# Optimization experiments

Hardware: AMD Instinct MI355X
Metric: run time of the kernel (lower is better)

Reference implementation:

```python
import jax, jax.numpy as jnp
import numpy as np

B, S, D = 4, 2048, 1024
H = 16
HD = D // H  # head dim = 64


def setup_inputs() -> dict:
    key = jax.random.key(0)
    ks = jax.random.split(key, 9)
    s = 1.0 / np.sqrt(D)
    return {
        "Q": jax.random.normal(ks[0], (B, S, D), dtype=jnp.float32),
        "K": jax.random.normal(ks[1], (B, S, D), dtype=jnp.float32),
        "V": jax.random.normal(ks[2], (B, S, D), dtype=jnp.float32),
        "Wq": jax.random.uniform(ks[3], (D, D), jnp.float32, -s, s),
        "bq": jax.random.uniform(ks[4], (D,), jnp.float32, -s, s),
        "Wk": jax.random.uniform(ks[5], (D, D), jnp.float32, -s, s),
        "bk": jax.random.uniform(ks[6], (D,), jnp.float32, -s, s),
        "Wv": jax.random.uniform(ks[7], (D, D), jnp.float32, -s, s),
        "bv": jax.random.uniform(ks[8], (D,), jnp.float32, -s, s),
    }


def reference(Q, K, V, Wq, bq, Wk, bk, Wv, bv):
    # Linear projections, split into heads: (B, H, S, HD)
    def proj(x, W, b):
        y = x @ W + b  # torch Linear uses x @ W.T; here W is stored pre-transposed (D_in, D_out)
        return y.reshape(B, S, H, HD).transpose(0, 2, 1, 3)

    q = proj(Q, Wq, bq)
    k = proj(K, Wk, bk)
    v = proj(V, Wv, bv)

    scale = 1.0 / jnp.sqrt(jnp.float32(HD))
    scores = jnp.einsum("bhqd,bhkd->bhqk", q, k) * scale  # (B,H,S,S)
    # causal mask (mask=True path): -inf above the diagonal
    causal = jnp.triu(jnp.full((S, S), -jnp.inf, dtype=scores.dtype), k=1)
    scores = scores + causal
    attn = jax.nn.softmax(scores, axis=-1)
    ctx = jnp.einsum("bhqk,bhkd->bhqd", attn, v)  # (B,H,S,HD)
    return ctx.transpose(0, 2, 1, 3).reshape(B, S, H * HD)
```

## Files before the change

kernel.cpp:

```cpp
#include <hip/hip_runtime.h>
#include <hip/hip_bf16.h>
#include <stdint.h>

#define B_  4
#define S_  2048
#define D_  1024
#define H_  16
#define HD_ 64
#define LOG2E 1.44269504088896f

typedef unsigned short u16;
typedef short bf16x8 __attribute__((ext_vector_type(8)));
typedef float f32x4 __attribute__((ext_vector_type(4)));

static __device__ __forceinline__ u16 f2bf(float f) {
    union { float f; uint32_t u; } v; v.f = f;
    return (u16)((v.u + 0x7FFF + ((v.u >> 16) & 1)) >> 16);
}

static __device__ __forceinline__ uint32_t cvt_pk_bf16(float lo, float hi) {
    uint32_t r;
    asm("v_cvt_pk_bf16_f32 %0, %1, %2" : "=v"(r) : "v"(lo), "v"(hi));
    return r;
}

static __device__ __forceinline__ uint32_t pk2(float lo, float hi) {
    return __builtin_amdgcn_perm(__float_as_uint(hi), __float_as_uint(lo), 0x07060302u);
}

static __device__ __forceinline__ bf16x8 rd_swz(const u16* base, int row, int slot) {
    return *(const bf16x8*)((const char*)base + row * 128 + ((slot ^ (row & 7)) << 4));
}

static __device__ __forceinline__ void gll_swz(const u16* grow0, size_t stride,
                                               u16* lds_chunk, int lane) {
    const int r = lane >> 3;
    const int slot = (lane & 7) ^ r;
    const u16* g = grow0 + (size_t)r * stride + slot * 8;
    __builtin_amdgcn_global_load_lds(
        (const __attribute__((address_space(1))) uint32_t*)g,
        (__attribute__((address_space(3))) uint32_t*)lds_chunk, 16, 0, 0);
}

__global__ __launch_bounds__(256) void wtrans(
    const float* __restrict__ W0, const float* __restrict__ W1, const float* __restrict__ W2,
    u16* __restrict__ T0, u16* __restrict__ T1, u16* __restrict__ T2)
{
    const float* W = blockIdx.z == 0 ? W0 : (blockIdx.z == 1 ? W1 : W2);
    u16* T       = blockIdx.z == 0 ? T0 : (blockIdx.z == 1 ? T1 : T2);
    __shared__ float t[32][33];
    const int n0 = blockIdx.x * 32, k0 = blockIdx.y * 32;
    const int tx = threadIdx.x, ty = threadIdx.y;
#pragma unroll
    for (int i = 0; i < 4; ++i)
        t[ty + i * 8][tx] = W[(size_t)(k0 + ty + i * 8) * D_ + n0 + tx];
    __syncthreads();
#pragma unroll
    for (int i = 0; i < 4; ++i)
        T[(size_t)(n0 + ty + i * 8) * D_ + k0 + tx] = f2bf(t[tx][ty + i * 8]);
}

template <int MODE>
__global__ __launch_bounds__(256) void proj_gemm(
    const float* __restrict__ X, const u16* __restrict__ Wt,
    const float* __restrict__ bias, u16* __restrict__ out)
{
    __shared__ __align__(16) u16 lA[2][128 * 64];
    __shared__ __align__(16) u16 lB[2][128 * 64];
    const int tid = threadIdx.x;
    const int m0 = blockIdx.x * 128, n0 = blockIdx.y * 128;
    const int w = tid >> 6, lane = tid & 63;
    const int lr = lane & 15, lg = lane >> 4;
    const int wr = (w >> 1) * 64, wc = (w & 1) * 64;

    f32x4 acc[4][4] = {};
    float4 areg[8];

    auto loadA = [&](int k0) {
#pragma unroll
        for (int i = 0; i < 4; ++i) {
            const int lin = (i * 256 + tid) * 8;
            const int r = lin >> 6, c = lin & 63;
            const float* p = X + (size_t)(m0 + r) * D_ + k0 + c;
            areg[2 * i]     = *(const float4*)p;
            areg[2 * i + 1] = *(const float4*)(p + 4);
        }
    };
    auto writeA = [&](u16* dst) {
#pragma unroll
        for (int i = 0; i < 4; ++i) {
            const int lin = (i * 256 + tid) * 8;
            const int r = lin >> 6, c = lin & 63;
            uint4 pk;
            pk.x = pk2(areg[2 * i].x,     areg[2 * i].y);
            pk.y = pk2(areg[2 * i].z,     areg[2 * i].w);
            pk.z = pk2(areg[2 * i + 1].x, areg[2 * i + 1].y);
            pk.w = pk2(areg[2 * i + 1].z, areg[2 * i + 1].w);
            const int phys = r * 128 + (((c >> 3) ^ (r & 7)) << 4);
            *(uint4*)((char*)dst + phys) = pk;
        }
    };
    auto stageB = [&](int k0, u16* dst) {
#pragma unroll
        for (int i = 0; i < 4; ++i) {
            const int c = w * 4 + i;
            gll_swz(Wt + (size_t)(n0 + c * 8) * D_ + k0, D_, dst + c * 512, lane);
        }
    };
    auto mfmaStep = [&](const u16* A, const u16* Bb) {
#pragma unroll
        for (int kk = 0; kk < 2; ++kk) {
            bf16x8 af[4], bfr[4];
#pragma unroll
            for (int m = 0; m < 4; ++m)
                af[m] = rd_swz(A, wr + m * 16 + lr, kk * 4 + lg);
#pragma unroll
            for (int n = 0; n < 4; ++n)
                bfr[n] = rd_swz(Bb, wc + n * 16 + lr, kk * 4 + lg);
#pragma unroll
            for (int m = 0; m < 4; ++m)
#pragma unroll
                for (int n = 0; n < 4; ++n)
                    acc[m][n] = __builtin_amdgcn_mfma_f32_16x16x32_bf16(af[m], bfr[n], acc[m][n], 0, 0, 0);
        }
    };

    loadA(0);
    stageB(0, lB[0]);
    writeA(lA[0]);
    __syncthreads();

    for (int k0 = 0, s = 0; k0 < D_; k0 += 64, s ^= 1) {
        const int nk = k0 + 64;
        if (nk < D_) {
            loadA(nk);
            stageB(nk, lB[s ^ 1]);
        }
        mfmaStep(lA[s], lB[s]);
        if (nk < D_) writeA(lA[s ^ 1]);
        __syncthreads();
    }

#pragma unroll
    for (int m = 0; m < 4; ++m)
#pragma unroll
        for (int n = 0; n < 4; ++n)
#pragma unroll
            for (int j = 0; j < 4; ++j) {
                const int gm = m0 + wr + m * 16 + lg * 4 + j;
                const int gn = n0 + wc + n * 16 + lr;
                float y = acc[m][n][j] + bias[gn];
                if (MODE == 0) y *= 0.125f * LOG2E;
                const int bb = gm >> 11, s2 = gm & (S_ - 1);
                const int h = gn >> 6, hd = gn & 63;
                size_t off;
                if (MODE < 2) off = (((size_t)bb * H_ + h) * S_ + s2) * HD_ + hd;
                else {
                    const int s6 = s2 & 63;
                    const int sp = (s2 & ~63) | (s6 & 0x20) | ((s6 & 0xC) << 1) |
                                   ((s6 & 0x10) >> 2) | (s6 & 3);
                    off = (((size_t)bb * H_ + h) * HD_ + hd) * S_ + sp;
                }
                out[off] = f2bf(y);
            }
}

__global__ __launch_bounds__(512) void attn_kernel(
    const u16* __restrict__ qb, const u16* __restrict__ kb,
    const u16* __restrict__ vtb, float* __restrict__ out)
{
    const int flat = (int)blockIdx.x;
    const int qA = flat >> 6;
    const int bh = ((flat & 7) << 3) | ((flat >> 3) & 7);
    const int b = bh >> 4, h = bh & 15;
    const int tid = threadIdx.x;
    const int w = tid >> 6, lane = tid & 63;
    const int lr = lane & 15, lg = lane >> 4;

    __shared__ __align__(16) u16 lds[2][4][64 * 64];

    const size_t kbase = (size_t)bh * S_ * HD_;
    const size_t vbase = (size_t)bh * HD_ * S_;

    union { uint32_t u[4]; bf16x8 v; } onesf;
    onesf.u[0] = onesf.u[1] = onesf.u[2] = onesf.u[3] = 0x3F803F80u;

    const int qB = 15 - qA;
    const int q0A = qA * 128, q0B = qB * 128;
    const int qrowA = q0A + w * 16 + lr;
    const int qrowB = q0B + w * 16 + lr;
    const int tmaxA = 2 * qA + 1, tmaxB = 2 * qB + 1;

    const size_t qoffA = ((size_t)bh * S_ + qrowA) * HD_;
    const size_t qoffB = ((size_t)bh * S_ + qrowB) * HD_;
    const bf16x8 qfA0 = *(const bf16x8*)(qb + qoffA + lg * 8);
    const bf16x8 qfA1 = *(const bf16x8*)(qb + qoffA + 32 + lg * 8);
    const bf16x8 qfB0 = *(const bf16x8*)(qb + qoffB + lg * 8);
    const bf16x8 qfB1 = *(const bf16x8*)(qb + qoffB + 32 + lg * 8);

    f32x4 oaccA[4] = {}, oaccB[4] = {};
    f32x4 laccA = {}, laccB = {};

    auto stage = [&](int tp, int s) {
        const int kvA = tp * 64, kvB = kvA + 64;
        u16* d = &lds[s][0][0];
        gll_swz(kb + kbase + (size_t)(kvA + w * 8) * HD_, HD_, d + w * 512, lane);
        gll_swz(vtb + vbase + (size_t)(w * 8) * S_ + kvA, S_, d + 4096 + w * 512, lane);
        gll_swz(kb + kbase + (size_t)(kvB + w * 8) * HD_, HD_, d + 8192 + w * 512, lane);
        gll_swz(vtb + vbase + (size_t)(w * 8) * S_ + kvB, S_, d + 12288 + w * 512, lane);
    };

    auto computeT = [&](int t, const u16* lK, const u16* lV,
                        const bf16x8& Qf0, const bf16x8& Qf1,
                        f32x4 (&oacc)[4], f32x4& lacc, int qrow, int tmax) {
        const int kv0 = t * 64;
        f32x4 sacc[4];
        __builtin_amdgcn_s_setprio(1);
#pragma unroll
        for (int n = 0; n < 4; ++n) {
            const bf16x8 k0f = rd_swz(lK, n * 16 + lr, lg);
            const bf16x8 k1f = rd_swz(lK, n * 16 + lr, 4 + lg);
            f32x4 z = {};
            z = __builtin_amdgcn_mfma_f32_16x16x32_bf16(k0f, Qf0, z, 0, 0, 0);
            z = __builtin_amdgcn_mfma_f32_16x16x32_bf16(k1f, Qf1, z, 0, 0, 0);
            sacc[n] = z;
        }
        __builtin_amdgcn_s_setprio(0);

        if (t >= tmax - 1) {
#pragma unroll
            for (int n = 0; n < 4; ++n)
#pragma unroll
                for (int j = 0; j < 4; ++j)
                    if (kv0 + n * 16 + lg * 4 + j > qrow) sacc[n][j] = -1e30f;
        }

        uint32_t pw[4][2];
#pragma unroll
        for (int n = 0; n < 4; ++n)
#pragma unroll
            for (int jh = 0; jh < 2; ++jh)
                pw[n][jh] = cvt_pk_bf16(exp2f(sacc[n][2 * jh]),
                                        exp2f(sacc[n][2 * jh + 1]));

        union { uint32_t u[4]; bf16x8 v; } a0, a1;
        a0.u[0] = pw[0][0]; a0.u[1] = pw[0][1];
        a0.u[2] = pw[1][0]; a0.u[3] = pw[1][1];
        a1.u[0] = pw[2][0]; a1.u[1] = pw[2][1];
        a1.u[2] = pw[3][0]; a1.u[3] = pw[3][1];

        __builtin_amdgcn_s_setprio(1);
#pragma unroll
        for (int n = 0; n < 4; ++n) {
            const int row = n * 16 + lr;
            const bf16x8 vf0 = rd_swz(lV, row, lg);
            const bf16x8 vf1 = rd_swz(lV, row, 4 + lg);
            oacc[n] = __builtin_amdgcn_mfma_f32_16x16x32_bf16(a0.v, vf0, oacc[n], 0, 0, 0);
            oacc[n] = __builtin_amdgcn_mfma_f32_16x16x32_bf16(a1.v, vf1, oacc[n], 0, 0, 0);
        }
        lacc = __builtin_amdgcn_mfma_f32_16x16x32_bf16(a0.v, onesf.v, lacc, 0, 0, 0);
        lacc = __builtin_amdgcn_mfma_f32_16x16x32_bf16(a1.v, onesf.v, lacc, 0, 0, 0);
        __builtin_amdgcn_s_setprio(0);
    };

    stage(0, 0);
    __syncthreads();

    for (int tp = 0, s = 0; tp <= tmaxB; tp += 2, s ^= 1) {
        if (tp + 2 <= tmaxB) stage(tp + 2, s ^ 1);
        const u16* base = &lds[s][0][0];

        computeT(tp, base, base + 4096, qfB0, qfB1, oaccB, laccB, qrowB, tmaxB);
        if (!(tp + 1 == tmaxB && w < 4))
            computeT(tp + 1, base + 8192, base + 12288, qfB0, qfB1, oaccB, laccB, qrowB, tmaxB);

        if (tp <= tmaxA) {
            computeT(tp, base, base + 4096, qfA0, qfA1, oaccA, laccA, qrowA, tmaxA);
            if (!(tp + 1 == tmaxA && w < 4))
                computeT(tp + 1, base + 8192, base + 12288, qfA0, qfA1, oaccA, laccA, qrowA, tmaxA);
        }
        __syncthreads();
    }

    {
        f32x4 inv;
#pragma unroll
        for (int j = 0; j < 4; ++j) inv[j] = 1.f / laccA[j];
#pragma unroll
        for (int j = 0; j < 4; ++j) {
            const int row = q0A + w * 16 + lg * 4 + j;
#pragma unroll
            for (int n = 0; n < 4; ++n)
                out[((size_t)b * S_ + row) * D_ + h * HD_ + n * 16 + lr] = oaccA[n][j] * inv[j];
        }
    }
    {
        f32x4 inv;
#pragma unroll
        for (int j = 0; j < 4; ++j) inv[j] = 1.f / laccB[j];
#pragma unroll
        for (int j = 0; j < 4; ++j) {
            const int row = q0B + w * 16 + lg * 4 + j;
#pragma unroll
            for (int n = 0; n < 4; ++n)
                out[((size_t)b * S_ + row) * D_ + h * HD_ + n * 16 + lr] = oaccB[n][j] * inv[j];
        }
    }
}

extern "C" void kernel_launch(void* const* d_in, const int* in_sizes, int n_in,
                              void* d_out, int out_size, void* d_ws, size_t ws_size,
                              hipStream_t stream) {
    const float* Q  = (const float*)d_in[0];
    const float* K  = (const float*)d_in[1];
    const float* V  = (const float*)d_in[2];
    const float* Wq = (const float*)d_in[3];
    const float* bq = (const float*)d_in[4];
    const float* Wk = (const float*)d_in[5];
    const float* bk = (const float*)d_in[6];
    const float* Wv = (const float*)d_in[7];
    const float* bv = (const float*)d_in[8];
    float* out = (float*)d_out;

    char* ws = (char*)d_ws;
    const size_t WT_BYTES  = (size_t)D_ * D_ * 2;
    const size_t QKV_BYTES = (size_t)B_ * S_ * D_ * 2;
    u16* Wtq = (u16*)(ws);
    u16* Wtk = (u16*)(ws + WT_BYTES);
    u16* Wtv = (u16*)(ws + 2 * WT_BYTES);
    u16* qb  = (u16*)(ws + 3 * WT_BYTES);
    u16* kb  = (u16*)(ws + 3 * WT_BYTES + QKV_BYTES);
    u16* vtb = (u16*)(ws + 3 * WT_BYTES + 2 * QKV_BYTES);

    wtrans<<<dim3(32, 32, 3), dim3(32, 8), 0, stream>>>(Wq, Wk, Wv, Wtq, Wtk, Wtv);
    proj_gemm<0><<<dim3(64, 8), dim3(256), 0, stream>>>(Q, Wtq, bq, qb);
    proj_gemm<1><<<dim3(64, 8), dim3(256), 0, stream>>>(K, Wtk, bk, kb);
    proj_gemm<2><<<dim3(64, 8), dim3(256), 0, stream>>>(V, Wtv, bv, vtb);
    attn_kernel<<<dim3(512), dim3(512), 0, stream>>>(qb, kb, vtb, out);
}
```

Baseline: 144.6 us.

## Deepen projection GEMM pipeline with register double-buffered A prefetch and partial vmcnt waits

```diff
diff --git a/kernel.cpp b/kernel.cpp
--- a/kernel.cpp
+++ b/kernel.cpp
@@ -59,6 +59,19 @@
     for (int i = 0; i < 4; ++i)
         T[(size_t)(n0 + ty + i * 8) * D_ + k0 + tx] = f2bf(t[tx][ty + i * 8]);
 }
+
+#define PIPE_BAR8() do {                                            \
+    asm volatile("s_waitcnt lgkmcnt(0)" ::: "memory");              \
+    asm volatile("s_waitcnt vmcnt(8)" ::: "memory");                \
+    __builtin_amdgcn_s_barrier();                                   \
+    __builtin_amdgcn_sched_barrier(0);                              \
+} while (0)
+#define PIPE_BAR0() do {                                            \
+    asm volatile("s_waitcnt lgkmcnt(0)" ::: "memory");              \
+    asm volatile("s_waitcnt vmcnt(0)" ::: "memory");                \
+    __builtin_amdgcn_s_barrier();                                   \
+    __builtin_amdgcn_sched_barrier(0);                              \
+} while (0)
 
 template <int MODE>
 __global__ __launch_bounds__(256) void proj_gemm(
@@ -74,9 +87,9 @@
     const int wr = (w >> 1) * 64, wc = (w & 1) * 64;
 
     f32x4 acc[4][4] = {};
-    float4 areg[8];
-
-    auto loadA = [&](int k0) {
+    float4 aregA[8], aregB[8];
+
+    auto loadA = [&](int k0, float4 (&areg)[8]) {
 #pragma unroll
         for (int i = 0; i < 4; ++i) {
             const int lin = (i * 256 + tid) * 8;
@@ -86,7 +99,7 @@
             areg[2 * i + 1] = *(const float4*)(p + 4);
         }
     };
-    auto writeA = [&](u16* dst) {
+    auto writeA = [&](const float4 (&areg)[8], u16* dst) {
 #pragma unroll
         for (int i = 0; i < 4; ++i) {
             const int lin = (i * 256 + tid) * 8;
@@ -125,20 +138,34 @@
         }
     };
 
-    loadA(0);
+    loadA(0, aregA);
     stageB(0, lB[0]);
-    writeA(lA[0]);
-    __syncthreads();
-
-    for (int k0 = 0, s = 0; k0 < D_; k0 += 64, s ^= 1) {
-        const int nk = k0 + 64;
-        if (nk < D_) {
-            loadA(nk);
-            stageB(nk, lB[s ^ 1]);
-        }
-        mfmaStep(lA[s], lB[s]);
-        if (nk < D_) writeA(lA[s ^ 1]);
-        __syncthreads();
+    writeA(aregA, lA[0]);
+    loadA(64, aregA);
+    PIPE_BAR8();
+
+#pragma unroll 1
+    for (int k0 = 0; k0 < D_; k0 += 128) {
+        {
+            const int nk1 = k0 + 64, nk2 = k0 + 128;
+            stageB(nk1, lB[1]);
+            if (nk2 < D_) loadA(nk2, aregB);
+            mfmaStep(lA[0], lB[0]);
+            writeA(aregA, lA[1]);
+            if (nk2 < D_) PIPE_BAR8(); else PIPE_BAR0();
+        }
+        {
+            const int nk1 = k0 + 128, nk2 = k0 + 192;
+            if (nk1 < D_) {
+                stageB(nk1, lB[0]);
+                if (nk2 < D_) loadA(nk2, aregA);
+                mfmaStep(lA[1], lB[1]);
+                writeA(aregB, lA[0]);
+                if (nk2 < D_) PIPE_BAR8(); else PIPE_BAR0();
+            } else {
+                mfmaStep(lA[1], lB[1]);
+            }
+        }
     }
 
 #pragma unroll
```

New measurement: 196.3 us. +35.7%, slower.
